# Kernel optimization log

Measured on AMD Instinct MI355X. Metric: run time of the kernel, lower is better.

## Reference

```python
import jax, jax.numpy as jnp
import numpy as np

N = 20000       # nodes
C = 64          # channels per irrep
E = 320000      # edges (avg degree 16)
S = 64          # num_species
R = 8           # radial embedding dim
HR = 64         # radial MLP hidden
HEADS = 2       # readout heads
AVG = 16.0      # avg_num_neighbors
SOFT = 2.0      # soft_normalization


def setup_inputs() -> dict:
    key = jax.random.key(0)
    ks = jax.random.split(key, 28)
    g = lambda k, sh, sc=1.0: jax.random.normal(k, sh, dtype=jnp.float32) * sc
    inv = lambda n: 1.0 / float(np.sqrt(n))
    return {
        "edge_vectors": g(ks[0], (E, 3)),
        "node_feats_s": g(ks[1], (N, C)),
        "node_feats_v": g(ks[2], (N, C, 3)),
        "radial_embeddings": g(ks[3], (E, R)),
        "node_species": jax.random.randint(ks[4], (N,), 0, S),
        "senders": jax.random.randint(ks[5], (E,), 0, N),
        "receivers": jax.random.randint(ks[6], (E,), 0, N),
        # residual FullyConnectedTensorProduct(feats, one-hot species) weights
        "W_rs": g(ks[7], (S, C, C), inv(C)),
        "W_rv": g(ks[8], (S, C, C), inv(C)),
        # interaction: linear up, radial MLP (5 TP paths), linear down
        "W_up_s": g(ks[9], (C, C), inv(C)),
        "W_up_v": g(ks[10], (C, C), inv(C)),
        "Wr1": g(ks[11], (R, HR), inv(R)),
        "Wr2": g(ks[12], (HR, 5 * C), inv(HR)),
        "W_down_s": g(ks[13], (C, C), inv(C)),
        "W_down_v": g(ks[14], (C, C), inv(C)),
        # equivariant product basis: per-channel species-indexed symmetric-contraction weights
        "w1s": g(ks[15], (S, C)),
        "w1v": g(ks[16], (S, C)),
        "w2ss": g(ks[17], (S, C)),
        "w2vv": g(ks[18], (S, C)),
        "w2sv": g(ks[19], (S, C)),
        "W_prod_s": g(ks[20], (C, C), inv(C)),
        "W_prod_v": g(ks[21], (C, C), inv(C)),
        # linear readout heads (out_irreps -> 1x0e per head)
        "w_read": g(ks[22], (HEADS, C), inv(C)),
    }


def reference(edge_vectors, node_feats_s, node_feats_v, radial_embeddings,
              node_species, senders, receivers,
              W_rs, W_rv, W_up_s, W_up_v, Wr1, Wr2, W_down_s, W_down_v,
              w1s, w1v, w2ss, w2vv, w2sv, W_prod_s, W_prod_v, w_read):
    n_nodes = node_feats_s.shape[0]
    sp = node_species

    # --- residual connection: FCTP(feats, one-hot(species)) == species-indexed channel mix
    res_s = jnp.einsum('nc,ncd->nd', node_feats_s, W_rs[sp])
    res_v = jnp.einsum('ncx,ncd->ndx', node_feats_v, W_rv[sp])

    # --- InteractionBlock ---
    s_u = node_feats_s @ W_up_s
    v_u = jnp.einsum('ncx,cd->ndx', node_feats_v, W_up_v)
    nrm = jnp.linalg.norm(edge_vectors, axis=-1, keepdims=True)
    u = edge_vectors / jnp.maximum(nrm, 1e-9)  # l=1 spherical harmonic direction [E,3]
    # radial MLP -> per-edge per-channel weights for the 5 CG paths of (0e+1o)x(0e+1o)->0e+1o
    w = (jax.nn.silu(radial_embeddings @ Wr1) @ Wr2).reshape(-1, 5, s_u.shape[1])
    se = s_u[senders]            # [E,C] gather (irregular)
    ve = v_u[senders]            # [E,C,3]
    dot = jnp.einsum('ecx,ex->ec', ve, u)          # 1o x 1o -> 0e
    crs = jnp.cross(ve, u[:, None, :])             # 1o x 1o -> 1o
    m_s = w[:, 0] * se + w[:, 3] * dot
    m_v = (w[:, 1][..., None] * ve
           + w[:, 2][..., None] * u[:, None, :]
           + w[:, 4][..., None] * crs)
    a_s = jax.ops.segment_sum(m_s, receivers, num_segments=n_nodes) / AVG
    a_v = jax.ops.segment_sum(m_v, receivers, num_segments=n_nodes) / AVG
    a_s = a_s @ W_down_s
    a_v = jnp.einsum('ncx,cd->ndx', a_v, W_down_v)

    # --- EquivariantProductBasisBlock: symmetric contraction (correlation<=2), per-channel
    # species-indexed weights, followed by a linear to out_irreps ---
    vv = jnp.sum(a_v * a_v, axis=-1)                                   # 1o (x) 1o -> 0e
    p_s = w1s[sp] * a_s + w2ss[sp] * a_s * a_s + w2vv[sp] * vv
    p_v = w1v[sp][..., None] * a_v + w2sv[sp][..., None] * a_s[..., None] * a_v
    p_s = p_s @ W_prod_s
    p_v = jnp.einsum('ncx,cd->ndx', p_v, W_prod_v)

    # --- soft normalization: phi(n) = 1/(1 + n*sus(n)), n = norm/SOFT ---
    def sus(x):
        return jnp.where(x > 0, jnp.exp(-1.0 / jnp.where(x > 0, x, 1.0)), 0.0)

    def phi(n):
        n = n / SOFT
        return 1.0 / (1.0 + n * sus(n))

    f_s = p_s * phi(jnp.abs(p_s))
    f_v = p_v * phi(jnp.linalg.norm(p_v, axis=-1, keepdims=True))

    # --- residual add ---
    f_s = f_s + res_s
    f_v = f_v + res_v

    # --- readout heads (Linear out_irreps -> 1x0e), stacked on axis=1 ---
    node_out = jnp.einsum('nc,hc->nh', f_s, w_read)
    return (node_out, f_s, f_v)
```

## Files before the change

### kernel.cpp

```cpp
#include <hip/hip_runtime.h>

#define N_NODES 20000
#define C 64
#define E_EDGES 320000
#define S_SPEC 64
#define R_DIM 8
#define HR 64
#define HEADS 2
#define NPAIR (E_EDGES/128)
#define HPAD 68
#define INV_AVG (1.0f/16.0f)

#define NB_WR2T 80
#define NB_WPACK 1056
#define NB_HIST 1250
#define NB_NODEUP 5000
#define PREP_BLOCKS (NB_WR2T + NB_WPACK + NB_HIST + NB_NODEUP)

#define FS_OFF 40000
#define FV_OFF 1320000

typedef short bf16x4 __attribute__((ext_vector_type(4)));
typedef float f32x4  __attribute__((ext_vector_type(4)));
typedef unsigned int uint2v __attribute__((ext_vector_type(2)));
typedef float f32x4e __attribute__((ext_vector_type(4)));

__device__ __forceinline__ unsigned short f2bf(float f){
  unsigned u = __float_as_uint(f);
  u += 0x7fffu + ((u >> 16) & 1u);
  return (unsigned short)(u >> 16);
}
__device__ __forceinline__ float bf2f(unsigned short b){
  return __uint_as_float(((unsigned)b) << 16);
}
__device__ __forceinline__ unsigned packbf(float a, float b){
  return (unsigned)f2bf(a) | ((unsigned)f2bf(b) << 16);
}
__device__ __forceinline__ float unplo(unsigned u){ return __uint_as_float(u << 16); }
__device__ __forceinline__ float unphi(unsigned u){ return __uint_as_float(u & 0xffff0000u); }
__device__ __forceinline__ float phi_f(float x){
  float n = x * 0.5f;
  float s = (n > 0.0f) ? expf(-1.0f/n) : 0.0f;
  return 1.0f / (1.0f + n * s);
}

__global__ __launch_bounds__(256) void prep_kernel(
    const float* __restrict__ Wr2, unsigned short* __restrict__ wr2t,
    const float* __restrict__ W_rs, const float* __restrict__ W_rv,
    const float* __restrict__ W_ds, const float* __restrict__ W_dv,
    const float* __restrict__ W_ps, const float* __restrict__ W_pv,
    unsigned* __restrict__ wrp, unsigned* __restrict__ wdp, unsigned* __restrict__ wpp,
    const int* __restrict__ rcv, int* __restrict__ count,
    const float* __restrict__ fs, const float* __restrict__ fv,
    const float* __restrict__ Wus, const float* __restrict__ Wuv,
    ushort4* __restrict__ suv)
{
  const int b = blockIdx.x;
  const int t = threadIdx.x;
  if (b < NB_WR2T){
    int idx = b*256 + t;
    int n = idx >> 6, k = idx & 63;
    wr2t[idx] = f2bf(Wr2[k*320 + n] * INV_AVG);
    return;
  }
  if (b < NB_WR2T + NB_WPACK){
    int idx = (b - NB_WR2T)*256 + t;
    if (idx < S_SPEC*C*C){
      wrp[idx] = packbf(W_rs[idx], W_rv[idx]);
    } else {
      int r2 = idx - S_SPEC*C*C;
      if (r2 < 4096) wdp[r2] = packbf(W_ds[r2], W_dv[r2]);
      else           wpp[r2-4096] = packbf(W_ps[r2-4096], W_pv[r2-4096]);
    }
    return;
  }
  if (b < NB_WR2T + NB_WPACK + NB_HIST){
    int e = (b - NB_WR2T - NB_WPACK)*256 + t;
    atomicAdd(&count[rcv[e]], 1);
    return;
  }
  {
    __shared__ float wus_l[C*C];
    __shared__ float wuv_l[C*C];
    __shared__ float s_l[4][C];
    __shared__ float v_l[4][3][C];
    const int nb = b - (NB_WR2T + NB_WPACK + NB_HIST);
    const int ni = t >> 6;
    const int d  = t & 63;
    const int n  = nb*4 + ni;
    #pragma unroll
    for (int j = 0; j < 16; ++j){
      wus_l[t + 256*j] = Wus[t + 256*j];
      wuv_l[t + 256*j] = Wuv[t + 256*j];
    }
    s_l[ni][d] = fs[n*C + d];
    #pragma unroll
    for (int x = 0; x < 3; ++x) v_l[ni][x][d] = fv[(n*C + d)*3 + x];
    __syncthreads();
    float as = 0.f, a0 = 0.f, a1 = 0.f, a2 = 0.f;
    #pragma unroll 4
    for (int c = 0; c < C; ++c){
      float wsv = wus_l[c*C + d];
      float wvv = wuv_l[c*C + d];
      as += s_l[ni][c] * wsv;
      a0 += v_l[ni][0][c] * wvv;
      a1 += v_l[ni][1][c] * wvv;
      a2 += v_l[ni][2][c] * wvv;
    }
    ushort4 o;
    o.x = f2bf(as); o.y = f2bf(a0); o.z = f2bf(a1); o.w = f2bf(a2);
    suv[(size_t)n*C + d] = o;
  }
}

__global__ __launch_bounds__(1024) void scan_kernel(const int* __restrict__ count, int* __restrict__ cursor){
  __shared__ int wsum[16];
  const int t = threadIdx.x;
  const int lane = t & 63, wid = t >> 6;
  const int base = t*20;
  int s = 0;
  int loc[20];
  #pragma unroll 4
  for (int i = 0; i < 20; ++i){
    int idx = base+i;
    int v = (idx < N_NODES) ? count[idx] : 0;
    loc[i] = v; s += v;
  }
  int x = s;
  #pragma unroll
  for (int dlt = 1; dlt < 64; dlt <<= 1){
    int y = __shfl_up(x, dlt);
    if (lane >= dlt) x += y;
  }
  if (lane == 63) wsum[wid] = x;
  __syncthreads();
  if (wid == 0 && lane < 16){
    int w = wsum[lane];
    #pragma unroll
    for (int dlt = 1; dlt < 16; dlt <<= 1){
      int y = __shfl_up(w, dlt);
      if (lane >= dlt) w += y;
    }
    wsum[lane] = w;
  }
  __syncthreads();
  int wpre = (wid > 0) ? wsum[wid-1] : 0;
  int run = wpre + (x - s);
  #pragma unroll 4
  for (int i = 0; i < 20; ++i){
    int idx = base+i;
    if (idx < N_NODES){ cursor[idx] = run; run += loc[i]; }
  }
}

__global__ __launch_bounds__(256) void scatter_kernel(
    const int* __restrict__ snd, const int* __restrict__ rcv,
    const float* __restrict__ ev, const float* __restrict__ re,
    int* __restrict__ cursor,
    int* __restrict__ snd_s, int* __restrict__ rcv_s,
    float4* __restrict__ u_s, float* __restrict__ re_s){
  int e = blockIdx.x*256 + threadIdx.x;
  int r = rcv[e];
  int pos = atomicAdd(&cursor[r], 1);
  snd_s[pos] = snd[e];
  rcv_s[pos] = r;
  float x = ev[e*3+0], y = ev[e*3+1], z = ev[e*3+2];
  float nr = sqrtf(x*x + y*y + z*z);
  float inv = 1.0f / fmaxf(nr, 1e-9f);
  float4 u4; u4.x = x*inv; u4.y = y*inv; u4.z = z*inv; u4.w = 0.f;
  u_s[pos] = u4;
  const float4* rp = (const float4*)&re[(size_t)e*R_DIM];
  float4 ra = rp[0], rb = rp[1];
  float4* op = (float4*)&re_s[(size_t)pos*R_DIM];
  op[0] = ra; op[1] = rb;
}

__global__ __launch_bounds__(512, 4) void edge_kernel(
    const float4* __restrict__ u_s, const float* __restrict__ re_s,
    const int* __restrict__ snd_s, const int* __restrict__ rcv_s,
    const float* __restrict__ Wr1, const unsigned short* __restrict__ wr2t,
    const ushort4* __restrict__ suv,
    float* __restrict__ a_s, float* __restrict__ a_v)
{
  __shared__ __align__(16) float Wr1_l[R_DIM*HR];
  __shared__ __align__(16) unsigned short Wr2T_l[320*HPAD];

  const int t = threadIdx.x;
  const int lane = t & 63;
  const int w = t >> 6;
  const int g  = w >> 1;
  const int h2 = w & 1;
  int b = blockIdx.x;
  int xcd = b & 7, idx = b >> 3;
  const int q = NPAIR >> 3, r = NPAIR & 7;
  int pair = (xcd < r ? xcd*(q+1) : r*(q+1) + (xcd-r)*q) + idx;
  const int e0A = pair * 128;
  const int e0B = e0A + 64;

  Wr1_l[t] = Wr1[t];
  #pragma unroll
  for (int j = 0; j < 10; ++j){
    int i4 = t + 512*j;
    uint2v v2 = __builtin_nontemporal_load((const uint2v*)wr2t + i4);
    int el = i4*4; int n = el >> 6, k = el & 63;
    *(uint2v*)&Wr2T_l[n*HPAD + k] = v2;
  }

  const int arow = g*16 + (lane & 15);
  const int koff = 4*(lane >> 4);
  const int cl = lane & 15;
  const int ebase = g*16 + (lane >> 4)*4;

  f32x4e raA = __builtin_nontemporal_load((const f32x4e*)&re_s[(size_t)(e0A + arow)*R_DIM]);
  f32x4e rbA = __builtin_nontemporal_load((const f32x4e*)&re_s[(size_t)(e0A + arow)*R_DIM] + 1);
  float uxA[4], uyA[4], uzA[4]; int snA[4], rcA[4];
  #pragma unroll
  for (int i = 0; i < 4; ++i){
    int e = e0A + ebase + i;
    f32x4e uu = __builtin_nontemporal_load((const f32x4e*)u_s + e);
    uxA[i]=uu.x; uyA[i]=uu.y; uzA[i]=uu.z;
    snA[i]=__builtin_nontemporal_load(snd_s + e);
    rcA[i]=__builtin_nontemporal_load(rcv_s + e);
  }
  uint2v gvA[4][2];
  #pragma unroll
  for (int i = 0; i < 4; ++i){
    const uint2v* sp_ = (const uint2v*)(suv + (size_t)snA[i]*C);
    #pragma unroll
    for (int kk = 0; kk < 2; ++kk)
      gvA[i][kk] = __builtin_nontemporal_load(sp_ + (2*h2 + kk)*16 + cl);
  }
  __syncthreads();

  bf16x4 haA[4];
  #pragma unroll
  for (int kt = 0; kt < 4; ++kt){
    short4 tmp;
    #pragma unroll
    for (int j = 0; j < 4; ++j){
      int k = kt*16 + koff + j;
      float acc = raA.x*Wr1_l[0*HR+k] + raA.y*Wr1_l[1*HR+k] + raA.z*Wr1_l[2*HR+k] + raA.w*Wr1_l[3*HR+k]
                + rbA.x*Wr1_l[4*HR+k] + rbA.y*Wr1_l[5*HR+k] + rbA.z*Wr1_l[6*HR+k] + rbA.w*Wr1_l[7*HR+k];
      float sil = acc / (1.0f + expf(-acc));
      ((unsigned short*)&tmp)[j] = f2bf(sil);
    }
    haA[kt] = *(bf16x4*)&tmp;
  }

  f32x4e raB = __builtin_nontemporal_load((const f32x4e*)&re_s[(size_t)(e0B + arow)*R_DIM]);
  f32x4e rbB = __builtin_nontemporal_load((const f32x4e*)&re_s[(size_t)(e0B + arow)*R_DIM] + 1);
  float uxB[4], uyB[4], uzB[4]; int snB[4], rcB[4];
  #pragma unroll
  for (int i = 0; i < 4; ++i){
    int e = e0B + ebase + i;
    f32x4e uu = __builtin_nontemporal_load((const f32x4e*)u_s + e);
    uxB[i]=uu.x; uyB[i]=uu.y; uzB[i]=uu.z;
    snB[i]=__builtin_nontemporal_load(snd_s + e);
    rcB[i]=__builtin_nontemporal_load(rcv_s + e);
  }

  f32x4 accA[10];
  #pragma unroll
  for (int lf = 0; lf < 10; ++lf) accA[lf] = (f32x4){0.f,0.f,0.f,0.f};
  #pragma unroll
  for (int kt = 0; kt < 4; ++kt){
    bf16x4 af = haA[kt];
    #pragma unroll
    for (int lf = 0; lf < 10; ++lf){
      int p = lf >> 1, kk = lf & 1;
      int n = (p*4 + 2*h2 + kk)*16 + cl;
      bf16x4 bf = *(const bf16x4*)&Wr2T_l[n*HPAD + kt*16 + koff];
      accA[lf] = __builtin_amdgcn_mfma_f32_16x16x16bf16_1k(af, bf, accA[lf], 0, 0, 0);
    }
  }

  uint2v gvB[4][2];
  #pragma unroll
  for (int i = 0; i < 4; ++i){
    const uint2v* sp_ = (const uint2v*)(suv + (size_t)snB[i]*C);
    #pragma unroll
    for (int kk = 0; kk < 2; ++kk)
      gvB[i][kk] = __builtin_nontemporal_load(sp_ + (2*h2 + kk)*16 + cl);
  }

  {
    float ms[2], mv0[2], mv1[2], mv2[2];
    #pragma unroll
    for (int kk = 0; kk < 2; ++kk){ ms[kk]=0.f; mv0[kk]=0.f; mv1[kk]=0.f; mv2[kk]=0.f; }
    int cur = rcA[0];
    #pragma unroll
    for (int i = 0; i < 4; ++i){
      int rc = rcA[i];
      if (rc != cur){
        #pragma unroll
        for (int kk = 0; kk < 2; ++kk){
          int c = (2*h2 + kk)*16 + cl;
          unsafeAtomicAdd(&a_s[cur*C + c],       ms[kk]);
          unsafeAtomicAdd(&a_v[(cur*3+0)*C + c], mv0[kk]);
          unsafeAtomicAdd(&a_v[(cur*3+1)*C + c], mv1[kk]);
          unsafeAtomicAdd(&a_v[(cur*3+2)*C + c], mv2[kk]);
          ms[kk]=0.f; mv0[kk]=0.f; mv1[kk]=0.f; mv2[kk]=0.f;
        }
        cur = rc;
      }
      float u0 = uxA[i], u1 = uyA[i], u2 = uzA[i];
      #pragma unroll
      for (int kk = 0; kk < 2; ++kk){
        float se  = unplo(gvA[i][kk].x);
        float ve0 = unphi(gvA[i][kk].x);
        float ve1 = unplo(gvA[i][kk].y);
        float ve2 = unphi(gvA[i][kk].y);
        float w0 = accA[0*2+kk][i];
        float w1 = accA[1*2+kk][i];
        float w2 = accA[2*2+kk][i];
        float w3 = accA[3*2+kk][i];
        float w4 = accA[4*2+kk][i];
        float dt  = ve0*u0 + ve1*u1 + ve2*u2;
        float cr0 = ve1*u2 - ve2*u1;
        float cr1 = ve2*u0 - ve0*u2;
        float cr2 = ve0*u1 - ve1*u0;
        ms[kk]  += w0*se + w3*dt;
        mv0[kk] += w1*ve0 + w2*u0 + w4*cr0;
        mv1[kk] += w1*ve1 + w2*u1 + w4*cr1;
        mv2[kk] += w1*ve2 + w2*u2 + w4*cr2;
      }
    }
    #pragma unroll
    for (int kk = 0; kk < 2; ++kk){
      int c = (2*h2 + kk)*16 + cl;
      unsafeAtomicAdd(&a_s[cur*C + c],       ms[kk]);
      unsafeAtomicAdd(&a_v[(cur*3+0)*C + c], mv0[kk]);
      unsafeAtomicAdd(&a_v[(cur*3+1)*C + c], mv1[kk]);
      unsafeAtomicAdd(&a_v[(cur*3+2)*C + c], mv2[kk]);
    }
  }

  bf16x4 haB[4];
  #pragma unroll
  for (int kt = 0; kt < 4; ++kt){
    short4 tmp;
    #pragma unroll
    for (int j = 0; j < 4; ++j){
      int k = kt*16 + koff + j;
      float acc = raB.x*Wr1_l[0*HR+k] + raB.y*Wr1_l[1*HR+k] + raB.z*Wr1_l[2*HR+k] + raB.w*Wr1_l[3*HR+k]
                + rbB.x*Wr1_l[4*HR+k] + rbB.y*Wr1_l[5*HR+k] + rbB.z*Wr1_l[6*HR+k] + rbB.w*Wr1_l[7*HR+k];
      float sil = acc / (1.0f + expf(-acc));
      ((unsigned short*)&tmp)[j] = f2bf(sil);
    }
    haB[kt] = *(bf16x4*)&tmp;
  }
  f32x4 accB[10];
  #pragma unroll
  for (int lf = 0; lf < 10; ++lf) accB[lf] = (f32x4){0.f,0.f,0.f,0.f};
  #pragma unroll
  for (int kt = 0; kt < 4; ++kt){
    bf16x4 af = haB[kt];
    #pragma unroll
    for (int lf = 0; lf < 10; ++lf){
      int p = lf >> 1, kk = lf & 1;
      int n = (p*4 + 2*h2 + kk)*16 + cl;
      bf16x4 bf = *(const bf16x4*)&Wr2T_l[n*HPAD + kt*16 + koff];
      accB[lf] = __builtin_amdgcn_mfma_f32_16x16x16bf16_1k(af, bf, accB[lf], 0, 0, 0);
    }
  }

  {
    float ms[2], mv0[2], mv1[2], mv2[2];
    #pragma unroll
    for (int kk = 0; kk < 2; ++kk){ ms[kk]=0.f; mv0[kk]=0.f; mv1[kk]=0.f; mv2[kk]=0.f; }
    int cur = rcB[0];
    #pragma unroll
    for (int i = 0; i < 4; ++i){
      int rc = rcB[i];
      if (rc != cur){
        #pragma unroll
        for (int kk = 0; kk < 2; ++kk){
          int c = (2*h2 + kk)*16 + cl;
          unsafeAtomicAdd(&a_s[cur*C + c],       ms[kk]);
          unsafeAtomicAdd(&a_v[(cur*3+0)*C + c], mv0[kk]);
          unsafeAtomicAdd(&a_v[(cur*3+1)*C + c], mv1[kk]);
          unsafeAtomicAdd(&a_v[(cur*3+2)*C + c], mv2[kk]);
          ms[kk]=0.f; mv0[kk]=0.f; mv1[kk]=0.f; mv2[kk]=0.f;
        }
        cur = rc;
      }
      float u0 = uxB[i], u1 = uyB[i], u2 = uzB[i];
      #pragma unroll
      for (int kk = 0; kk < 2; ++kk){
        float se  = unplo(gvB[i][kk].x);
        float ve0 = unphi(gvB[i][kk].x);
        float ve1 = unplo(gvB[i][kk].y);
        float ve2 = unphi(gvB[i][kk].y);
        float w0 = accB[0*2+kk][i];
        float w1 = accB[1*2+kk][i];
        float w2 = accB[2*2+kk][i];
        float w3 = accB[3*2+kk][i];
        float w4 = accB[4*2+kk][i];
        float dt  = ve0*u0 + ve1*u1 + ve2*u2;
        float cr0 = ve1*u2 - ve2*u1;
        float cr1 = ve2*u0 - ve0*u2;
        float cr2 = ve0*u1 - ve1*u0;
        ms[kk]  += w0*se + w3*dt;
        mv0[kk] += w1*ve0 + w2*u0 + w4*cr0;
        mv1[kk] += w1*ve1 + w2*u1 + w4*cr1;
        mv2[kk] += w1*ve2 + w2*u2 + w4*cr2;
      }
    }
    #pragma unroll
    for (int kk = 0; kk < 2; ++kk){
      int c = (2*h2 + kk)*16 + cl;
      unsafeAtomicAdd(&a_s[cur*C + c],       ms[kk]);
      unsafeAtomicAdd(&a_v[(cur*3+0)*C + c], mv0[kk]);
      unsafeAtomicAdd(&a_v[(cur*3+1)*C + c], mv1[kk]);
      unsafeAtomicAdd(&a_v[(cur*3+2)*C + c], mv2[kk]);
    }
  }
}

__global__ __launch_bounds__(256) void node_post_kernel(
    const float* __restrict__ a_s, const float* __restrict__ a_v,
    const float* __restrict__ fs_in, const float* __restrict__ fv_in,
    const int* __restrict__ species,
    const unsigned* __restrict__ wrp,
    const unsigned* __restrict__ wdp,
    const unsigned* __restrict__ wpp,
    const float* __restrict__ w1s, const float* __restrict__ w1v,
    const float* __restrict__ w2ss, const float* __restrict__ w2vv, const float* __restrict__ w2sv,
    const float* __restrict__ w_read, float* __restrict__ out)
{
  const int ni = threadIdx.x >> 6;
  const int d  = threadIdx.x & 63;
  const int n  = blockIdx.x*4 + ni;
  const int sp = species[n];
  const int t  = threadIdx.x;
  __shared__ float as_l[4][C];
  __shared__ float av_l[4][3][C];
  __shared__ float si_l[4][C];
  __shared__ float vi_l[4][3][C];
  __shared__ unsigned wdp_l[C*C];
  __shared__ unsigned wpp_l[C*C];
  #pragma unroll
  for (int j = 0; j < 16; ++j){
    wdp_l[t + 256*j] = wdp[t + 256*j];
    wpp_l[t + 256*j] = wpp[t + 256*j];
  }
  as_l[ni][d] = a_s[n*C + d];
  #pragma unroll
  for (int x=0;x<3;x++) av_l[ni][x][d] = a_v[(n*3+x)*C + d];
  si_l[ni][d] = fs_in[n*C + d];
  #pragma unroll
  for (int x=0;x<3;x++) vi_l[ni][x][d] = fv_in[(n*C + d)*3 + x];
  __syncthreads();
  const unsigned* wrp_p = wrp + (size_t)sp*C*C;
  float bs=0, bv0=0, bv1=0, bv2=0, rs=0, rv0=0, rv1=0, rv2=0;
  #pragma unroll 4
  for (int c=0;c<C;++c){
    unsigned ud = wdp_l[c*C+d];
    unsigned ur = wrp_p[c*C+d];
    float wds = unplo(ud), wdv = unphi(ud);
    float wrs = unplo(ur), wrv = unphi(ur);
    bs  += as_l[ni][c]*wds;
    bv0 += av_l[ni][0][c]*wdv; bv1 += av_l[ni][1][c]*wdv; bv2 += av_l[ni][2][c]*wdv;
    rs  += si_l[ni][c]*wrs;
    rv0 += vi_l[ni][0][c]*wrv; rv1 += vi_l[ni][1][c]*wrv; rv2 += vi_l[ni][2][c]*wrv;
  }
  float vv = bv0*bv0 + bv1*bv1 + bv2*bv2;
  float ps  = w1s[sp*C+d]*bs + w2ss[sp*C+d]*bs*bs + w2vv[sp*C+d]*vv;
  float c1v = w1v[sp*C+d], c2sv = w2sv[sp*C+d];
  float pv0 = c1v*bv0 + c2sv*bs*bv0;
  float pv1 = c1v*bv1 + c2sv*bs*bv1;
  float pv2 = c1v*bv2 + c2sv*bs*bv2;
  __syncthreads();
  as_l[ni][d] = ps; av_l[ni][0][d]=pv0; av_l[ni][1][d]=pv1; av_l[ni][2][d]=pv2;
  __syncthreads();
  float qs=0, qv0=0, qv1=0, qv2=0;
  #pragma unroll 4
  for (int c=0;c<C;++c){
    unsigned up = wpp_l[c*C+d];
    float wps = unplo(up), wpv = unphi(up);
    qs  += as_l[ni][c]*wps;
    qv0 += av_l[ni][0][c]*wpv; qv1 += av_l[ni][1][c]*wpv; qv2 += av_l[ni][2][c]*wpv;
  }
  float fsv = qs * phi_f(fabsf(qs)) + rs;
  float nv = sqrtf(qv0*qv0 + qv1*qv1 + qv2*qv2);
  float ph = phi_f(nv);
  float fv0 = qv0*ph + rv0;
  float fv1 = qv1*ph + rv1;
  float fv2 = qv2*ph + rv2;
  out[FS_OFF + n*C + d] = fsv;
  float* fvo = &out[FV_OFF + (size_t)(n*C + d)*3];
  fvo[0]=fv0; fvo[1]=fv1; fvo[2]=fv2;
  #pragma unroll
  for (int h=0; h<HEADS; ++h){
    float r = fsv * w_read[h*C + d];
    #pragma unroll
    for (int off=32; off>0; off>>=1) r += __shfl_down(r, off);
    if (d == 0) out[n*HEADS + h] = r;
  }
}

extern "C" void kernel_launch(void* const* d_in, const int* in_sizes, int n_in,
                              void* d_out, int out_size, void* d_ws, size_t ws_size,
                              hipStream_t stream)
{
  const float* ev   = (const float*)d_in[0];
  const float* nfs  = (const float*)d_in[1];
  const float* nfv  = (const float*)d_in[2];
  const float* re   = (const float*)d_in[3];
  const int*   spec = (const int*)d_in[4];
  const int*   snd  = (const int*)d_in[5];
  const int*   rcv  = (const int*)d_in[6];
  const float* W_rs = (const float*)d_in[7];
  const float* W_rv = (const float*)d_in[8];
  const float* Wus  = (const float*)d_in[9];
  const float* Wuv  = (const float*)d_in[10];
  const float* Wr1  = (const float*)d_in[11];
  const float* Wr2  = (const float*)d_in[12];
  const float* Wds  = (const float*)d_in[13];
  const float* Wdv  = (const float*)d_in[14];
  const float* w1s  = (const float*)d_in[15];
  const float* w1v  = (const float*)d_in[16];
  const float* w2ss = (const float*)d_in[17];
  const float* w2vv = (const float*)d_in[18];
  const float* w2sv = (const float*)d_in[19];
  const float* Wps  = (const float*)d_in[20];
  const float* Wpv  = (const float*)d_in[21];
  const float* wrd  = (const float*)d_in[22];

  float* out = (float*)d_out;
  float* ws  = (float*)d_ws;
  ushort4* suv  = (ushort4*)ws;
  float*   a_s  = ws + 2560000;
  float*   a_v  = ws + 3840000;
  int*    count = (int*)(ws + 7680000);
  int*    cursr = (int*)(ws + 7700000);
  int*    snd_s = (int*)(ws + 7720000);
  int*    rcv_s = (int*)(ws + 8040000);
  float4* u_s   = (float4*)(ws + 8360000);
  float*  re_s  = ws + 9640000;
  unsigned short* wr2t = (unsigned short*)(ws + 12200000);
  unsigned* wrp = (unsigned*)(ws + 12210240);
  unsigned* wdp = (unsigned*)(ws + 12472384);
  unsigned* wpp = (unsigned*)(ws + 12476480);

  hipMemsetAsync(a_s, 0, (size_t)5120000*sizeof(float), stream);
  hipMemsetAsync(count, 0, (size_t)N_NODES*sizeof(int), stream);

  prep_kernel<<<PREP_BLOCKS, 256, 0, stream>>>(
      Wr2, wr2t, W_rs, W_rv, Wds, Wdv, Wps, Wpv, wrp, wdp, wpp,
      rcv, count, nfs, nfv, Wus, Wuv, suv);
  scan_kernel<<<1, 1024, 0, stream>>>(count, cursr);
  scatter_kernel<<<E_EDGES/256, 256, 0, stream>>>(snd, rcv, ev, re, cursr,
                                                  snd_s, rcv_s, u_s, re_s);
  edge_kernel<<<NPAIR, 512, 0, stream>>>(u_s, re_s, snd_s, rcv_s, Wr1, wr2t,
                                         suv, a_s, a_v);
  node_post_kernel<<<N_NODES/4, 256, 0, stream>>>(a_s, a_v, nfs, nfv, spec,
      wrp, wdp, wpp, w1s, w1v, w2ss, w2vv, w2sv, wrd, out);
}
```

Baseline: 388.5 us.

## Amortize weight staging over more nodes per block and drop nontemporal loads

```diff
diff --git a/kernel.cpp b/kernel.cpp
--- a/kernel.cpp
+++ b/kernel.cpp
@@ -14,7 +14,7 @@
 #define NB_WR2T 80
 #define NB_WPACK 1056
 #define NB_HIST 1250
-#define NB_NODEUP 5000
+#define NB_NODEUP 2500
 #define PREP_BLOCKS (NB_WR2T + NB_WPACK + NB_HIST + NB_NODEUP)
 
 #define FS_OFF 40000
@@ -22,8 +22,6 @@
 
 typedef short bf16x4 __attribute__((ext_vector_type(4)));
 typedef float f32x4  __attribute__((ext_vector_type(4)));
-typedef unsigned int uint2v __attribute__((ext_vector_type(2)));
-typedef float f32x4e __attribute__((ext_vector_type(4)));
 
 __device__ __forceinline__ unsigned short f2bf(float f){
   unsigned u = __float_as_uint(f);
@@ -87,29 +85,33 @@
     const int nb = b - (NB_WR2T + NB_WPACK + NB_HIST);
     const int ni = t >> 6;
     const int d  = t & 63;
-    const int n  = nb*4 + ni;
     #pragma unroll
     for (int j = 0; j < 16; ++j){
       wus_l[t + 256*j] = Wus[t + 256*j];
       wuv_l[t + 256*j] = Wuv[t + 256*j];
     }
-    s_l[ni][d] = fs[n*C + d];
-    #pragma unroll
-    for (int x = 0; x < 3; ++x) v_l[ni][x][d] = fv[(n*C + d)*3 + x];
-    __syncthreads();
-    float as = 0.f, a0 = 0.f, a1 = 0.f, a2 = 0.f;
-    #pragma unroll 4
-    for (int c = 0; c < C; ++c){
-      float wsv = wus_l[c*C + d];
-      float wvv = wuv_l[c*C + d];
-      as += s_l[ni][c] * wsv;
-      a0 += v_l[ni][0][c] * wvv;
-      a1 += v_l[ni][1][c] * wvv;
-      a2 += v_l[ni][2][c] * wvv;
-    }
-    ushort4 o;
-    o.x = f2bf(as); o.y = f2bf(a0); o.z = f2bf(a1); o.w = f2bf(a2);
-    suv[(size_t)n*C + d] = o;
+    #pragma unroll
+    for (int pass = 0; pass < 2; ++pass){
+      const int n = nb*8 + pass*4 + ni;
+      s_l[ni][d] = fs[n*C + d];
+      #pragma unroll
+      for (int x = 0; x < 3; ++x) v_l[ni][x][d] = fv[(n*C + d)*3 + x];
+      __syncthreads();
+      float as = 0.f, a0 = 0.f, a1 = 0.f, a2 = 0.f;
+      #pragma unroll 4
+      for (int c = 0; c < C; ++c){
+        float wsv = wus_l[c*C + d];
+        float wvv = wuv_l[c*C + d];
+        as += s_l[ni][c] * wsv;
+        a0 += v_l[ni][0][c] * wvv;
+        a1 += v_l[ni][1][c] * wvv;
+        a2 += v_l[ni][2][c] * wvv;
+      }
+      ushort4 o;
+      o.x = f2bf(as); o.y = f2bf(a0); o.z = f2bf(a1); o.w = f2bf(a2);
+      suv[(size_t)n*C + d] = o;
+      __syncthreads();
+    }
   }
 }
 
@@ -201,9 +203,9 @@
   #pragma unroll
   for (int j = 0; j < 10; ++j){
     int i4 = t + 512*j;
-    uint2v v2 = __builtin_nontemporal_load((const uint2v*)wr2t + i4);
+    ushort4 v4 = ((const ushort4*)wr2t)[i4];
     int el = i4*4; int n = el >> 6, k = el & 63;
-    *(uint2v*)&Wr2T_l[n*HPAD + k] = v2;
+    *(ushort4*)&Wr2T_l[n*HPAD + k] = v4;
   }
 
   const int arow = g*16 + (lane & 15);
@@ -211,24 +213,22 @@
   const int cl = lane & 15;
   const int ebase = g*16 + (lane >> 4)*4;
 
-  f32x4e raA = __builtin_nontemporal_load((const f32x4e*)&re_s[(size_t)(e0A + arow)*R_DIM]);
-  f32x4e rbA = __builtin_nontemporal_load((const f32x4e*)&re_s[(size_t)(e0A + arow)*R_DIM] + 1);
+  float4 raA = ((const float4*)&re_s[(size_t)(e0A + arow)*R_DIM])[0];
+  float4 rbA = ((const float4*)&re_s[(size_t)(e0A + arow)*R_DIM])[1];
   float uxA[4], uyA[4], uzA[4]; int snA[4], rcA[4];
   #pragma unroll
   for (int i = 0; i < 4; ++i){
     int e = e0A + ebase + i;
-    f32x4e uu = __builtin_nontemporal_load((const f32x4e*)u_s + e);
+    float4 uu = u_s[e];
     uxA[i]=uu.x; uyA[i]=uu.y; uzA[i]=uu.z;
-    snA[i]=__builtin_nontemporal_load(snd_s + e);
-    rcA[i]=__builtin_nontemporal_load(rcv_s + e);
-  }
-  uint2v gvA[4][2];
+    snA[i]=snd_s[e]; rcA[i]=rcv_s[e];
+  }
+  ushort4 gvA[4][2];
   #pragma unroll
   for (int i = 0; i < 4; ++i){
-    const uint2v* sp_ = (const uint2v*)(suv + (size_t)snA[i]*C);
-    #pragma unroll
-    for (int kk = 0; kk < 2; ++kk)
-      gvA[i][kk] = __builtin_nontemporal_load(sp_ + (2*h2 + kk)*16 + cl);
+    const ushort4* sp_ = &suv[(size_t)snA[i]*C];
+    #pragma unroll
+    for (int kk = 0; kk < 2; ++kk) gvA[i][kk] = sp_[(2*h2 + kk)*16 + cl];
   }
   __syncthreads();
 
@@ -247,16 +247,15 @@
     haA[kt] = *(bf16x4*)&tmp;
   }
 
-  f32x4e raB = __builtin_nontemporal_load((const f32x4e*)&re_s[(size_t)(e0B + arow)*R_DIM]);
-  f32x4e rbB = __builtin_nontemporal_load((const f32x4e*)&re_s[(size_t)(e0B + arow)*R_DIM] + 1);
+  float4 raB = ((const float4*)&re_s[(size_t)(e0B + arow)*R_DIM])[0];
+  float4 rbB = ((const float4*)&re_s[(size_t)(e0B + arow)*R_DIM])[1];
   float uxB[4], uyB[4], uzB[4]; int snB[4], rcB[4];
   #pragma unroll
   for (int i = 0; i < 4; ++i){
     int e = e0B + ebase + i;
-    f32x4e uu = __builtin_nontemporal_load((const f32x4e*)u_s + e);
+    float4 uu = u_s[e];
     uxB[i]=uu.x; uyB[i]=uu.y; uzB[i]=uu.z;
-    snB[i]=__builtin_nontemporal_load(snd_s + e);
-    rcB[i]=__builtin_nontemporal_load(rcv_s + e);
+    snB[i]=snd_s[e]; rcB[i]=rcv_s[e];
   }
 
   f32x4 accA[10];
@@ -274,13 +273,12 @@
     }
   }
 
-  uint2v gvB[4][2];
+  ushort4 gvB[4][2];
   #pragma unroll
   for (int i = 0; i < 4; ++i){
-    const uint2v* sp_ = (const uint2v*)(suv + (size_t)snB[i]*C);
-    #pragma unroll
-    for (int kk = 0; kk < 2; ++kk)
-      gvB[i][kk] = __builtin_nontemporal_load(sp_ + (2*h2 + kk)*16 + cl);
+    const ushort4* sp_ = &suv[(size_t)snB[i]*C];
+    #pragma unroll
+    for (int kk = 0; kk < 2; ++kk) gvB[i][kk] = sp_[(2*h2 + kk)*16 + cl];
   }
 
   {
@@ -306,10 +304,10 @@
       float u0 = uxA[i], u1 = uyA[i], u2 = uzA[i];
       #pragma unroll
       for (int kk = 0; kk < 2; ++kk){
-        float se  = unplo(gvA[i][kk].x);
-        float ve0 = unphi(gvA[i][kk].x);
-        float ve1 = unplo(gvA[i][kk].y);
-        float ve2 = unphi(gvA[i][kk].y);
+        float se  = bf2f(gvA[i][kk].x);
+        float ve0 = bf2f(gvA[i][kk].y);
+        float ve1 = bf2f(gvA[i][kk].z);
+        float ve2 = bf2f(gvA[i][kk].w);
         float w0 = accA[0*2+kk][i];
         float w1 = accA[1*2+kk][i];
         float w2 = accA[2*2+kk][i];
@@ -387,10 +385,10 @@
       float u0 = uxB[i], u1 = uyB[i], u2 = uzB[i];
       #pragma unroll
       for (int kk = 0; kk < 2; ++kk){
-        float se  = unplo(gvB[i][kk].x);
-        float ve0 = unphi(gvB[i][kk].x);
-        float ve1 = unplo(gvB[i][kk].y);
-        float ve2 = unphi(gvB[i][kk].y);
+        float se  = bf2f(gvB[i][kk].x);
+        float ve0 = bf2f(gvB[i][kk].y);
+        float ve1 = bf2f(gvB[i][kk].z);
+        float ve2 = bf2f(gvB[i][kk].w);
         float w0 = accB[0*2+kk][i];
         float w1 = accB[1*2+kk][i];
         float w2 = accB[2*2+kk][i];
@@ -417,7 +415,7 @@
   }
 }
 
-__global__ __launch_bounds__(256) void node_post_kernel(
+__global__ __launch_bounds__(512) void node_post_kernel(
     const float* __restrict__ a_s, const float* __restrict__ a_v,
     const float* __restrict__ fs_in, const float* __restrict__ fv_in,
     const int* __restrict__ species,
@@ -430,19 +428,19 @@
 {
   const int ni = threadIdx.x >> 6;
   const int d  = threadIdx.x & 63;
-  const int n  = blockIdx.x*4 + ni;
+  const int n  = blockIdx.x*8 + ni;
   const int sp = species[n];
   const int t  = threadIdx.x;
-  __shared__ float as_l[4][C];
-  __shared__ float av_l[4][3][C];
-  __shared__ float si_l[4][C];
-  __shared__ float vi_l[4][3][C];
+  __shared__ float as_l[8][C];
+  __shared__ float av_l[8][3][C];
+  __shared__ float si_l[8][C];
+  __shared__ float vi_l[8][3][C];
   __shared__ unsigned wdp_l[C*C];
   __shared__ unsigned wpp_l[C*C];
   #pragma unroll
-  for (int j = 0; j < 16; ++j){
-    wdp_l[t + 256*j] = wdp[t + 256*j];
-    wpp_l[t + 256*j] = wpp[t + 256*j];
+  for (int j = 0; j < 8; ++j){
+    wdp_l[t + 512*j] = wdp[t + 512*j];
+    wpp_l[t + 512*j] = wpp[t + 512*j];
   }
   as_l[ni][d] = a_s[n*C + d];
   #pragma unroll
@@ -554,6 +552,6 @@
                                                   snd_s, rcv_s, u_s, re_s);
   edge_kernel<<<NPAIR, 512, 0, stream>>>(u_s, re_s, snd_s, rcv_s, Wr1, wr2t,
                                          suv, a_s, a_v);
-  node_post_kernel<<<N_NODES/4, 256, 0, stream>>>(a_s, a_v, nfs, nfv, spec,
+  node_post_kernel<<<N_NODES/8, 512, 0, stream>>>(a_s, a_v, nfs, nfv, spec,
       wrp, wdp, wpp, w1s, w1v, w2ss, w2vv, w2sv, wrd, out);
 }
```

Result: faster. 378.7 us (-2.5%).
